# Performance work log

Measured on AMD Instinct MI355X. Metric: run time of the kernel, lower is better.

The kernel has to match this reference:

```python
import jax, jax.numpy as jnp
import numpy as np

B, S, D = 8, 4096, 256
N_INTENT, N_SLOT = 512, 1024


def setup_inputs() -> dict:
    key = jax.random.key(0)
    k1, k2, k3, k4 = jax.random.split(key, 4)
    return {
        "input_intent": jax.random.normal(k1, (B, S, D), dtype=jnp.float32),
        "input_slot": jax.random.normal(k2, (B, S, D), dtype=jnp.float32),
        "mask": jnp.ones((B, S), dtype=jnp.int32),  # unused, kept for API fidelity
        "W_intent_emb": jax.random.normal(k3, (N_INTENT, D), dtype=jnp.float32) * 0.02,
        "W_slot_emb": jax.random.normal(k4, (N_SLOT, D), dtype=jnp.float32) * 0.02,
    }


def reference(input_intent, input_slot, mask, W_intent_emb, W_slot_emb):
    # scores: [B, S, N] = hidden @ label_table^T
    intent_probs = jax.nn.softmax(jnp.einsum("bsd,nd->bsn", input_intent, W_intent_emb), axis=-1)
    slot_probs = jax.nn.softmax(jnp.einsum("bsd,nd->bsn", input_slot, W_slot_emb), axis=-1)
    # weighted sum over label embeddings: [B, S, D]
    intent_res = jnp.einsum("bsn,nd->bsd", intent_probs, W_intent_emb)
    slot_res = jnp.einsum("bsn,nd->bsd", slot_probs, W_slot_emb)
    return (intent_res, slot_res)
```

## Files before the change

kernel.cpp:

```cpp
#include <hip/hip_runtime.h>


#define TM 128
#define DD 256
#define THREADS 512
#define TOK 32768

typedef __bf16 bf16t;
typedef bf16t v8bf __attribute__((ext_vector_type(8)));
typedef float v16f __attribute__((ext_vector_type(16)));

#define WT0   0
#define WT1   32768
#define P_OFF 65536
#define L_OFF 81920
#define LDS_BYTES 82432

#define IWT 0
#define SWT 262144
#define IW2 786432
#define SW2 1048576

__device__ __forceinline__ unsigned short f2bf(float x) {
    unsigned u = __builtin_bit_cast(unsigned, x);
    unsigned r = u + 0x7fffu + ((u >> 16) & 1u);
    return (unsigned short)(r >> 16);
}

__global__ __launch_bounds__(256) void prep_w_kernel(
    const float* __restrict__ w_int, const float* __restrict__ w_slot,
    char* __restrict__ wsb)
{
    int t = blockIdx.x * 256 + threadIdx.x;
    int w = t >> 6, lane = t & 63;
    int hi = lane >> 5, l5 = lane & 31;
    union { unsigned short u[8]; uint4 q; } pk;

    if (w < 768) {
        int st   = (w >= 256);
        int widx = w - (st ? 256 : 0);
        int it = widx >> 5, fid = widx & 31;
        int wc = fid >> 4, kk = fid & 15;
        const float* W = st ? w_slot : w_int;
        int n  = it * 64 + wc * 32 + l5;
        int k0 = kk * 16 + hi * 8;
        #pragma unroll
        for (int j = 0; j < 8; ++j) pk.u[j] = f2bf(W[(size_t)n * DD + k0 + j]);
        char* dst = wsb + (st ? SWT : IWT) + (size_t)it * 32768 + fid * 1024 + lane * 16;
        *(uint4*)dst = pk.q;
    } else {
        int w2 = w - 768;
        int st   = (w2 >= 256);
        int widx = w2 - (st ? 256 : 0);
        int it = widx >> 5, fid = widx & 31;
        int kb = fid >> 3, db = fid & 7;
        const float* W = st ? w_slot : w_int;
        int n0 = it * 64 + kb * 16 + hi * 8;
        int d  = db * 32 + l5;
        #pragma unroll
        for (int j = 0; j < 8; ++j) pk.u[j] = f2bf(W[(size_t)(n0 + j) * DD + d]);
        char* dst = wsb + (st ? SW2 : IW2) + (size_t)it * 32768 + fid * 1024 + lane * 16;
        *(uint4*)dst = pk.q;
    }
}

__global__ __launch_bounds__(THREADS, 2) void label_attn_kernel(
    const float* __restrict__ in_intent,
    const float* __restrict__ in_slot,
    const char* __restrict__ wsb,
    float* __restrict__ out)
{
    extern __shared__ char lds[];

    const int tid  = threadIdx.x;
    const int lane = tid & 63;
    const int wid  = tid >> 6;
    const int wr   = wid >> 1;
    const int wc   = wid & 1;
    const int hi   = lane >> 5;
    const int l5   = lane & 31;
    const int t0   = blockIdx.x * TM;

    float* lsf = (float*)(lds + L_OFF);

    const float* inps[2] = {in_intent, in_slot};
    const char*  wtb[2]  = {wsb + IWT, wsb + SWT};
    const char*  w2b[2]  = {wsb + IW2, wsb + SW2};
    const int    nits[2] = {8, 16};

    const int kbl_w = (l5 >> 4) & 1;
    const int hb_w  = (l5 >> 3) & 1;
    const int pw_base = P_OFF + wr * 4096 + (wc * 2 + kbl_w) * 1024 + (l5 & 7) * 2;
    const int pw_sxor = (kbl_w << 2) ^ (hb_w << 1);

    for (int st = 0; st < 2; ++st) {
        __builtin_amdgcn_s_barrier();
        if (tid < TM) lsf[tid] = 0.0f;

        const float* __restrict__ inp = inps[st];
        const char*  __restrict__ wtg = wtb[st];
        const char*  __restrict__ w2g = w2b[st];
        const int niter = nits[st];
        float* __restrict__ outp = out + (size_t)st * TOK * DD;

        v8bf h[16];
        {
            const float* hp = inp + (size_t)(t0 + wr * 32 + l5) * DD + hi * 8;
            #pragma unroll
            for (int kk = 0; kk < 16; ++kk) {
                float4 a = *(const float4*)(hp + kk * 16);
                float4 b = *(const float4*)(hp + kk * 16 + 4);
                union { unsigned short u[8]; v8bf v; } pk;
                pk.u[0] = f2bf(a.x); pk.u[1] = f2bf(a.y);
                pk.u[2] = f2bf(a.z); pk.u[3] = f2bf(a.w);
                pk.u[4] = f2bf(b.x); pk.u[5] = f2bf(b.y);
                pk.u[6] = f2bf(b.z); pk.u[7] = f2bf(b.w);
                h[kk] = pk.v;
            }
        }

        #pragma unroll
        for (int c = 0; c < 4; ++c) {
            int chunk = wid * 4 + c;
            __builtin_amdgcn_global_load_lds(
                (const __attribute__((address_space(1))) unsigned*)(wtg + chunk * 1024 + lane * 16),
                (__attribute__((address_space(3))) unsigned*)(lds + WT0 + chunk * 1024),
                16, 0, 0);
        }
        __builtin_amdgcn_sched_barrier(0);

        v8bf ring[16];
        #pragma unroll
        for (int kb = 0; kb < 4; ++kb)
            #pragma unroll
            for (int db = 0; db < 4; ++db)
                ring[kb * 4 + db] =
                    *(const v8bf*)(w2g + (kb * 8 + wc * 4 + db) * 1024 + lane * 16);

        v16f  o[4] = {};
        float ls[16] = {};

        asm volatile("s_waitcnt vmcnt(16)" ::: "memory");
        __builtin_amdgcn_sched_barrier(0);
        __builtin_amdgcn_s_barrier();

        for (int it = 0; it < niter; ++it) {
            char* wbuf = lds + ((it & 1) ? WT1 : WT0);

            if (it + 1 < niter) {
                char* nbuf = lds + ((it & 1) ? WT0 : WT1);
                const char* src = wtg + (size_t)(it + 1) * 32768;
                #pragma unroll
                for (int c = 0; c < 4; ++c) {
                    int chunk = wid * 4 + c;
                    __builtin_amdgcn_global_load_lds(
                        (const __attribute__((address_space(1))) unsigned*)(src + chunk * 1024 + lane * 16),
                        (__attribute__((address_space(3))) unsigned*)(nbuf + chunk * 1024),
                        16, 0, 0);
                }
            }

            v16f cacc = {};
            #pragma unroll
            for (int kk = 0; kk < 16; ++kk) {
                v8bf b1 = *(const v8bf*)(wbuf + (wc * 16 + kk) * 1024 + lane * 16);
                cacc = __builtin_amdgcn_mfma_f32_32x32x16_bf16(h[kk], b1, cacc, 0, 0, 0);
            }

            #pragma unroll
            for (int r = 0; r < 16; ++r) {
                int tl = (r & 3) + 8 * (r >> 2) + 4 * hi;
                float e = __expf(cacc[r]);
                unsigned short ub = f2bf(e);
                ls[r] += __builtin_bit_cast(float, ((unsigned)ub) << 16);
                int slot = (tl + 32 * hb_w) ^ pw_sxor;
                *(unsigned short*)(lds + pw_base + slot * 16) = ub;
            }

            asm volatile("s_waitcnt lgkmcnt(0)" ::: "memory");
            __builtin_amdgcn_sched_barrier(0);
            __builtin_amdgcn_s_barrier();

            #pragma unroll
            for (int kb = 0; kb < 4; ++kb) {
                int sl = lane ^ ((kb & 1) << 2) ^ (hi << 1);
                v8bf pa = *(const v8bf*)(lds + P_OFF + wr * 4096 + kb * 1024 + sl * 16);
                #pragma unroll
                for (int db = 0; db < 4; ++db)
                    o[db] = __builtin_amdgcn_mfma_f32_32x32x16_bf16(pa, ring[kb * 4 + db], o[db], 0, 0, 0);
            }

            if (it + 1 < niter) {
                const char* src = w2g + (size_t)(it + 1) * 32768;
                #pragma unroll
                for (int kb = 0; kb < 4; ++kb)
                    #pragma unroll
                    for (int db = 0; db < 4; ++db)
                        ring[kb * 4 + db] =
                            *(const v8bf*)(src + (kb * 8 + wc * 4 + db) * 1024 + lane * 16);
            }

            asm volatile("s_waitcnt vmcnt(16)" ::: "memory");
            __builtin_amdgcn_sched_barrier(0);
            __builtin_amdgcn_s_barrier();
        }

        #pragma unroll
        for (int r = 0; r < 16; ++r) {
            float s = ls[r];
            s += __shfl_xor(s, 1);
            s += __shfl_xor(s, 2);
            s += __shfl_xor(s, 4);
            s += __shfl_xor(s, 8);
            s += __shfl_xor(s, 16);
            ls[r] = s;
        }
        if (l5 == 0) {
            #pragma unroll
            for (int r = 0; r < 16; ++r) {
                int tl = (r & 3) + 8 * (r >> 2) + 4 * hi;
                atomicAdd(&lsf[wr * 32 + tl], ls[r]);
            }
        }
        __syncthreads();

        #pragma unroll
        for (int r = 0; r < 16; ++r) {
            int tl = (r & 3) + 8 * (r >> 2) + 4 * hi;
            float inv = 1.0f / lsf[wr * 32 + tl];
            size_t row = (size_t)(t0 + wr * 32 + tl);
            #pragma unroll
            for (int db = 0; db < 4; ++db)
                outp[row * DD + wc * 128 + db * 32 + l5] = o[db][r] * inv;
        }
    }
}

extern "C" void kernel_launch(void* const* d_in, const int* in_sizes, int n_in,
                              void* d_out, int out_size, void* d_ws, size_t ws_size,
                              hipStream_t stream) {
    const float* in_intent = (const float*)d_in[0];
    const float* in_slot   = (const float*)d_in[1];
    const float* w_intent  = (const float*)d_in[3];
    const float* w_slot    = (const float*)d_in[4];
    float* out = (float*)d_out;
    char* wsb = (char*)d_ws;

    (void)hipFuncSetAttribute((const void*)label_attn_kernel,
                              hipFuncAttributeMaxDynamicSharedMemorySize, LDS_BYTES);

    prep_w_kernel<<<384, 256, 0, stream>>>(w_intent, w_slot, wsb);

    label_attn_kernel<<<dim3(TOK / TM, 1, 1), dim3(THREADS, 1, 1), LDS_BYTES, stream>>>(
        in_intent, in_slot, wsb, out);
}
```

Measured before the change: 217.2 us.

## Stage second-GEMM weights through double-buffered LDS instead of register ring

The W2 weight tiles for the second matmul are now prefetched with global_load_lds into a double-buffered LDS region, replacing the 16-register ring filled by direct global loads. Wait counts are adjusted so each iteration's W1 and W2 prefetches overlap compute. The first GEMM is split into two independent accumulator chains to shorten the MFMA dependency chain. LDS use grows to about 148KB, and launch bounds become an explicit waves_per_eu(2,2) hint. Together these free registers but add LDS reads and may limit occupancy.

```diff
diff --git a/kernel.cpp b/kernel.cpp
--- a/kernel.cpp
+++ b/kernel.cpp
@@ -12,9 +12,11 @@
 
 #define WT0   0
 #define WT1   32768
-#define P_OFF 65536
-#define L_OFF 81920
-#define LDS_BYTES 82432
+#define W20   65536
+#define W21   98304
+#define P_OFF 131072
+#define L_OFF 147456
+#define LDS_BYTES 147968
 
 #define IWT 0
 #define SWT 262144
@@ -64,7 +66,9 @@
     }
 }
 
-__global__ __launch_bounds__(THREADS, 2) void label_attn_kernel(
+__global__ __launch_bounds__(THREADS)
+__attribute__((amdgpu_waves_per_eu(2, 2)))
+void label_attn_kernel(
     const float* __restrict__ in_intent,
     const float* __restrict__ in_slot,
     const char* __restrict__ wsb,
@@ -83,11 +87,6 @@
 
     float* lsf = (float*)(lds + L_OFF);
 
-    const float* inps[2] = {in_intent, in_slot};
-    const char*  wtb[2]  = {wsb + IWT, wsb + SWT};
-    const char*  w2b[2]  = {wsb + IW2, wsb + SW2};
-    const int    nits[2] = {8, 16};
-
     const int kbl_w = (l5 >> 4) & 1;
     const int hb_w  = (l5 >> 3) & 1;
     const int pw_base = P_OFF + wr * 4096 + (wc * 2 + kbl_w) * 1024 + (l5 & 7) * 2;
@@ -97,10 +96,10 @@
         __builtin_amdgcn_s_barrier();
         if (tid < TM) lsf[tid] = 0.0f;
 
-        const float* __restrict__ inp = inps[st];
-        const char*  __restrict__ wtg = wtb[st];
-        const char*  __restrict__ w2g = w2b[st];
-        const int niter = nits[st];
+        const float* __restrict__ inp = st ? in_slot : in_intent;
+        const char*  __restrict__ wtg = wsb + (st ? SWT : IWT);
+        const char*  __restrict__ w2g = wsb + (st ? SW2 : IW2);
+        const int niter = st ? 16 : 8;
         float* __restrict__ outp = out + (size_t)st * TOK * DD;
 
         v8bf h[16];
@@ -128,44 +127,61 @@
                 16, 0, 0);
         }
         __builtin_amdgcn_sched_barrier(0);
-
-        v8bf ring[16];
-        #pragma unroll
-        for (int kb = 0; kb < 4; ++kb)
-            #pragma unroll
-            for (int db = 0; db < 4; ++db)
-                ring[kb * 4 + db] =
-                    *(const v8bf*)(w2g + (kb * 8 + wc * 4 + db) * 1024 + lane * 16);
+        #pragma unroll
+        for (int c = 0; c < 4; ++c) {
+            int chunk = wid * 4 + c;
+            __builtin_amdgcn_global_load_lds(
+                (const __attribute__((address_space(1))) unsigned*)(w2g + chunk * 1024 + lane * 16),
+                (__attribute__((address_space(3))) unsigned*)(lds + W20 + chunk * 1024),
+                16, 0, 0);
+        }
+        __builtin_amdgcn_sched_barrier(0);
+        asm volatile("s_waitcnt vmcnt(0)" ::: "memory");
+        __builtin_amdgcn_sched_barrier(0);
+        __builtin_amdgcn_s_barrier();
 
         v16f  o[4] = {};
         float ls[16] = {};
 
-        asm volatile("s_waitcnt vmcnt(16)" ::: "memory");
-        __builtin_amdgcn_sched_barrier(0);
-        __builtin_amdgcn_s_barrier();
-
         for (int it = 0; it < niter; ++it) {
-            char* wbuf = lds + ((it & 1) ? WT1 : WT0);
+            const int cur = it & 1;
+            char* wt_buf = lds + (cur ? WT1 : WT0);
+            char* w2_buf = lds + (cur ? W21 : W20);
 
             if (it + 1 < niter) {
-                char* nbuf = lds + ((it & 1) ? WT0 : WT1);
-                const char* src = wtg + (size_t)(it + 1) * 32768;
+                const char* s1 = wtg + (size_t)(it + 1) * 32768;
+                const char* s2 = w2g + (size_t)(it + 1) * 32768;
+                char* d1 = lds + (cur ? WT0 : WT1);
+                char* d2 = lds + (cur ? W20 : W21);
                 #pragma unroll
                 for (int c = 0; c < 4; ++c) {
                     int chunk = wid * 4 + c;
                     __builtin_amdgcn_global_load_lds(
-                        (const __attribute__((address_space(1))) unsigned*)(src + chunk * 1024 + lane * 16),
-                        (__attribute__((address_space(3))) unsigned*)(nbuf + chunk * 1024),
+                        (const __attribute__((address_space(1))) unsigned*)(s1 + chunk * 1024 + lane * 16),
+                        (__attribute__((address_space(3))) unsigned*)(d1 + chunk * 1024),
                         16, 0, 0);
                 }
-            }
-
-            v16f cacc = {};
-            #pragma unroll
-            for (int kk = 0; kk < 16; ++kk) {
-                v8bf b1 = *(const v8bf*)(wbuf + (wc * 16 + kk) * 1024 + lane * 16);
-                cacc = __builtin_amdgcn_mfma_f32_32x32x16_bf16(h[kk], b1, cacc, 0, 0, 0);
-            }
+                __builtin_amdgcn_sched_barrier(0);
+                #pragma unroll
+                for (int c = 0; c < 4; ++c) {
+                    int chunk = wid * 4 + c;
+                    __builtin_amdgcn_global_load_lds(
+                        (const __attribute__((address_space(1))) unsigned*)(s2 + chunk * 1024 + lane * 16),
+                        (__attribute__((address_space(3))) unsigned*)(d2 + chunk * 1024),
+                        16, 0, 0);
+                }
+                __builtin_amdgcn_sched_barrier(0);
+            }
+
+            v16f c0 = {}, c1 = {};
+            #pragma unroll
+            for (int kk = 0; kk < 16; kk += 2) {
+                v8bf b0 = *(const v8bf*)(wt_buf + (wc * 16 + kk) * 1024 + lane * 16);
+                v8bf b1 = *(const v8bf*)(wt_buf + (wc * 16 + kk + 1) * 1024 + lane * 16);
+                c0 = __builtin_amdgcn_mfma_f32_32x32x16_bf16(h[kk],     b0, c0, 0, 0, 0);
+                c1 = __builtin_amdgcn_mfma_f32_32x32x16_bf16(h[kk + 1], b1, c1, 0, 0, 0);
+            }
+            v16f cacc = c0 + c1;
 
             #pragma unroll
             for (int r = 0; r < 16; ++r) {
@@ -177,6 +193,11 @@
                 *(unsigned short*)(lds + pw_base + slot * 16) = ub;
             }
 
+            if (it + 1 < niter) {
+                asm volatile("s_waitcnt vmcnt(8)" ::: "memory");
+            } else {
+                asm volatile("s_waitcnt vmcnt(0)" ::: "memory");
+            }
             asm volatile("s_waitcnt lgkmcnt(0)" ::: "memory");
             __builtin_amdgcn_sched_barrier(0);
             __builtin_amdgcn_s_barrier();
@@ -186,21 +207,15 @@
                 int sl = lane ^ ((kb & 1) << 2) ^ (hi << 1);
                 v8bf pa = *(const v8bf*)(lds + P_OFF + wr * 4096 + kb * 1024 + sl * 16);
                 #pragma unroll
-                for (int db = 0; db < 4; ++db)
-                    o[db] = __builtin_amdgcn_mfma_f32_32x32x16_bf16(pa, ring[kb * 4 + db], o[db], 0, 0, 0);
+                for (int db = 0; db < 4; ++db) {
+                    v8bf wb = *(const v8bf*)(w2_buf + (kb * 8 + wc * 4 + db) * 1024 + lane * 16);
+                    o[db] = __builtin_amdgcn_mfma_f32_32x32x16_bf16(pa, wb, o[db], 0, 0, 0);
+                }
             }
 
             if (it + 1 < niter) {
-                const char* src = w2g + (size_t)(it + 1) * 32768;
-                #pragma unroll
-                for (int kb = 0; kb < 4; ++kb)
-                    #pragma unroll
-                    for (int db = 0; db < 4; ++db)
-                        ring[kb * 4 + db] =
-                            *(const v8bf*)(src + (kb * 8 + wc * 4 + db) * 1024 + lane * 16);
-            }
-
-            asm volatile("s_waitcnt vmcnt(16)" ::: "memory");
+                asm volatile("s_waitcnt vmcnt(4)" ::: "memory");
+            }
             __builtin_amdgcn_sched_barrier(0);
             __builtin_amdgcn_s_barrier();
         }
```

After: 179.3 us. -17.4%, faster.
